# Kernel tuning notes

Hardware: AMD Instinct MI355X
Metric: run time of the kernel (lower is better)

Reference implementation:

```python
import jax, jax.numpy as jnp
import numpy as np

B, S, M, H = 4, 512, 128, 768
KEY_SIZE, VALUE_SIZE = 30000, 10000


def setup_inputs() -> dict:
    key = jax.random.key(0)
    k1, k2, k3, k4, k5, k6 = jax.random.split(key, 6)
    return {
        "word_seq": jax.random.randint(k1, (B, M), 0, KEY_SIZE),
        "hidden_state": jax.random.normal(k2, (B, S, H), dtype=jnp.float32),
        "label_value_matrix": jax.random.randint(k3, (B, S, M), 0, VALUE_SIZE),
        "word_mask_metrix": jax.random.uniform(k4, (B, S, M), dtype=jnp.float32),
        "key_table": jax.random.normal(k5, (KEY_SIZE, H), dtype=jnp.float32) * 0.02,
        "value_table": jax.random.normal(k6, (VALUE_SIZE, H), dtype=jnp.float32) * 0.02,
    }


def reference(word_seq, hidden_state, label_value_matrix, word_mask_metrix,
              key_table, value_table):
    temper = jnp.asarray(H, hidden_state.dtype) ** 0.5
    emb_a = key_table[word_seq]                      # [B, M, H]
    # u[b,s,m] = <hidden_state[b,s], emb_a[b,m]> / sqrt(H)
    u = jnp.einsum('bsh,bmh->bsm', hidden_state, emb_a) / temper
    mask = jnp.clip(word_mask_metrix, 0.0, 1.0)      # [B, S, M]
    delta_exp_u = jnp.exp(u) * mask                  # masked unnormalized attn
    p = delta_exp_u / (jnp.sum(delta_exp_u, axis=2, keepdims=True) + 1e-10)
    emb_c = value_table[label_value_matrix]          # [B, S, M, H]
    # o[b,s,h] = sum_m p[b,s,m] * emb_c[b,s,m,h]
    o = jnp.einsum('bsm,bsmh->bsh', p, emb_c)
    return o
```

## Files before the change

kernel.cpp:

```cpp
#include <hip/hip_runtime.h>
#include <hip/hip_bf16.h>


constexpr int B = 4, S = 512, M = 128, H = 768;
constexpr int C4 = H / 4;
constexpr int KEY_SIZE = 30000, VALUE_SIZE = 10000;

constexpr int VT_N = VALUE_SIZE * H;
constexpr int KA_N = B * M * H;
constexpr int HS_N = B * S * H;
constexpr int U_N  = B * S * M;

constexpr size_t VT_BYTES = (size_t)VT_N * 2;
constexpr size_t KA_BYTES = (size_t)KA_N * 2;
constexpr size_t HS_BYTES = (size_t)HS_N * 2;
constexpr size_t U_BYTES  = (size_t)U_N  * 4;
constexpr size_t WS_NEEDED = VT_BYTES + KA_BYTES + HS_BYTES + U_BYTES;

constexpr int VT_V4 = VT_N / 4, KA_V4 = KA_N / 4, HS_V4 = HS_N / 4;
constexpr int CONV_TOTAL = VT_V4 + KA_V4 + HS_V4;

typedef short  bf16x8  __attribute__((ext_vector_type(8)));
typedef float  floatx4 __attribute__((ext_vector_type(4)));

__device__ inline unsigned short f2bf(float f) {
    __hip_bfloat16 h = __float2bfloat16(f);
    return *reinterpret_cast<unsigned short*>(&h);
}
__device__ inline float bf2f(unsigned short u) {
    return __uint_as_float((unsigned)u << 16);
}
__device__ inline float4 bf4_to_f4(ushort4 u) {
    float4 f;
    f.x = bf2f(u.x); f.y = bf2f(u.y); f.z = bf2f(u.z); f.w = bf2f(u.w);
    return f;
}
__device__ inline ushort4 f4_to_bf4(float4 f) {
    ushort4 u; u.x = f2bf(f.x); u.y = f2bf(f.y); u.z = f2bf(f.z); u.w = f2bf(f.w);
    return u;
}

__global__ __launch_bounds__(256) void convert_kernel(
    const float* __restrict__ vt, const float* __restrict__ kt,
    const float* __restrict__ hs, const int* __restrict__ wseq,
    unsigned short* __restrict__ vt_bf, unsigned short* __restrict__ ka_bf,
    unsigned short* __restrict__ hs_bf)
{
    int i = blockIdx.x * 256 + threadIdx.x;
    if (i < VT_V4) {
        ((ushort4*)vt_bf)[i] = f4_to_bf4(((const float4*)vt)[i]);
    } else if (i < VT_V4 + KA_V4) {
        int j   = i - VT_V4;
        int c   = j % (H / 4);
        int row = j / (H / 4);
        int src = wseq[row];
        float4 f = ((const float4*)(kt + (size_t)src * H))[c];
        ((ushort4*)ka_bf)[j] = f4_to_bf4(f);
    } else if (i < CONV_TOTAL) {
        int j = i - VT_V4 - KA_V4;
        ((ushort4*)hs_bf)[j] = f4_to_bf4(((const float4*)hs)[j]);
    }
}

__global__ __launch_bounds__(256) void phaseA_kernel(
    const unsigned short* __restrict__ hs_bf,
    const unsigned short* __restrict__ ka_bf,
    float* __restrict__ u_ws)
{
    const int lane = threadIdx.x & 63;
    const int wave = threadIdx.x >> 6;
    const int tile = blockIdx.x * 4 + wave;
    const int b    = tile >> 8;
    const int r    = tile & 255;
    const int s0   = (r >> 3) << 4;
    const int m0   = (r & 7) << 4;
    const int l15  = lane & 15;
    const int quad = lane >> 4;

    const unsigned short* arow = hs_bf + (size_t)(b * S + s0 + l15) * H + quad * 8;
    const unsigned short* brow = ka_bf + (size_t)(b * M + m0 + l15) * H + quad * 8;

    floatx4 acc = {0.f, 0.f, 0.f, 0.f};
    #pragma unroll 4
    for (int k = 0; k < H; k += 32) {
        bf16x8 af = *(const bf16x8*)(arow + k);
        bf16x8 bf = *(const bf16x8*)(brow + k);
        acc = __builtin_amdgcn_mfma_f32_16x16x32_bf16(af, bf, acc, 0, 0, 0);
    }
    float* up = u_ws + (size_t)(b * S + s0 + quad * 4) * M + m0 + l15;
    up[0 * M] = acc[0];
    up[1 * M] = acc[1];
    up[2 * M] = acc[2];
    up[3 * M] = acc[3];
}

constexpr int GW = 6;
__global__ __launch_bounds__(384) void gather_kernel(
    const float* __restrict__ u_ws,
    const int*   __restrict__ lvm,
    const float* __restrict__ mask,
    const unsigned short* __restrict__ vt_bf,
    float*       __restrict__ out)
{
    const int bs   = blockIdx.x;
    const int t    = threadIdx.x;
    const int lane = t & 63;
    const int wave = t >> 6;

    __shared__ float  delta_s[M];
    __shared__ int    row_s[M];
    __shared__ float4 obuf[GW][C4];
    __shared__ float  dsum_s[GW];

    const float inv_temper = rsqrtf((float)H);
    if (t < M) {
        float u  = u_ws[(size_t)bs * M + t];
        float mk = mask[(size_t)bs * M + t];
        mk = fminf(fmaxf(mk, 0.f), 1.f);
        delta_s[t] = __expf(u * inv_temper) * mk;
        row_s[t]   = lvm[(size_t)bs * M + t];
    }
    __syncthreads();

    float4 a0 = {0.f,0.f,0.f,0.f}, a1 = {0.f,0.f,0.f,0.f}, a2 = {0.f,0.f,0.f,0.f};
    float dsum = 0.f;

    #pragma unroll 4
    for (int m = wave; m < M; m += GW) {
        const float pm = delta_s[m];
        const ushort4* vr = (const ushort4*)(vt_bf + (size_t)row_s[m] * H);
        const ushort4 vu0 = vr[lane];
        const ushort4 vu1 = vr[lane + 64];
        const ushort4 vu2 = vr[lane + 128];
        dsum += pm;
        const float4 v0 = bf4_to_f4(vu0);
        const float4 v1 = bf4_to_f4(vu1);
        const float4 v2 = bf4_to_f4(vu2);
        a0.x += pm*v0.x; a0.y += pm*v0.y; a0.z += pm*v0.z; a0.w += pm*v0.w;
        a1.x += pm*v1.x; a1.y += pm*v1.y; a1.z += pm*v1.z; a1.w += pm*v1.w;
        a2.x += pm*v2.x; a2.y += pm*v2.y; a2.z += pm*v2.z; a2.w += pm*v2.w;
    }

    obuf[wave][lane]       = a0;
    obuf[wave][lane + 64]  = a1;
    obuf[wave][lane + 128] = a2;
    if (lane == 0) dsum_s[wave] = dsum;
    __syncthreads();

    if (t < C4) {
        float d = 1e-10f;
        #pragma unroll
        for (int w = 0; w < GW; ++w) d += dsum_s[w];
        const float inv_d = 1.0f / d;
        float4 r = {0.f, 0.f, 0.f, 0.f};
        #pragma unroll
        for (int w = 0; w < GW; ++w) {
            const float4 o = obuf[w][t];
            r.x += o.x; r.y += o.y; r.z += o.z; r.w += o.w;
        }
        r.x *= inv_d; r.y *= inv_d; r.z *= inv_d; r.w *= inv_d;
        ((float4*)(out + (size_t)bs * H))[t] = r;
    }
}

__global__ __launch_bounds__(192) void kvmn_fp32_kernel(
    const int*   __restrict__ word_seq,
    const float* __restrict__ hidden_state,
    const int*   __restrict__ lvm,
    const float* __restrict__ mask,
    const float* __restrict__ key_table,
    const float* __restrict__ value_table,
    float*       __restrict__ out)
{
    const int bs   = blockIdx.x;
    const int b    = bs / S;
    const int t    = threadIdx.x;
    const int lane = t & 63;
    const int wave = t >> 6;

    __shared__ float4 hs4_s[C4];
    __shared__ int    wseq_s[M];
    __shared__ int    row_s[M];
    __shared__ float  mask_s[M];
    __shared__ float4 obuf[3][C4];
    __shared__ float  dsum_s[3];

    const float4* hs_g4 = (const float4*)(hidden_state + (size_t)bs * H);
    hs4_s[t] = hs_g4[t];
    if (t < M) {
        wseq_s[t] = word_seq[b * M + t];
        row_s[t]  = lvm[(size_t)bs * M + t];
        float mk  = mask[(size_t)bs * M + t];
        mask_s[t] = fminf(fmaxf(mk, 0.f), 1.f);
    }
    __syncthreads();

    const float4 h0 = hs4_s[lane];
    const float4 h1 = hs4_s[lane + 64];
    const float4 h2 = hs4_s[lane + 128];
    const float inv_temper = rsqrtf((float)H);
    const float4* kt4 = (const float4*)key_table;
    const float4* vt4 = (const float4*)value_table;

    float4 a0 = {0.f,0.f,0.f,0.f}, a1 = {0.f,0.f,0.f,0.f}, a2 = {0.f,0.f,0.f,0.f};
    float dsum = 0.f;

    #pragma unroll 2
    for (int m = wave; m < M; m += 3) {
        const float4* kr = kt4 + (size_t)wseq_s[m] * C4;
        const float4* vr = vt4 + (size_t)row_s[m]  * C4;
        const float4 k0 = kr[lane], k1 = kr[lane+64], k2 = kr[lane+128];
        const float4 v0 = vr[lane], v1 = vr[lane+64], v2 = vr[lane+128];
        float dot = h0.x*k0.x + h0.y*k0.y + h0.z*k0.z + h0.w*k0.w
                  + h1.x*k1.x + h1.y*k1.y + h1.z*k1.z + h1.w*k1.w
                  + h2.x*k2.x + h2.y*k2.y + h2.z*k2.z + h2.w*k2.w;
        #pragma unroll
        for (int off = 1; off < 64; off <<= 1) dot += __shfl_xor(dot, off);
        const float delta = __expf(dot * inv_temper) * mask_s[m];
        dsum += delta;
        a0.x += delta*v0.x; a0.y += delta*v0.y; a0.z += delta*v0.z; a0.w += delta*v0.w;
        a1.x += delta*v1.x; a1.y += delta*v1.y; a1.z += delta*v1.z; a1.w += delta*v1.w;
        a2.x += delta*v2.x; a2.y += delta*v2.y; a2.z += delta*v2.z; a2.w += delta*v2.w;
    }
    obuf[wave][lane] = a0; obuf[wave][lane+64] = a1; obuf[wave][lane+128] = a2;
    if (lane == 0) dsum_s[wave] = dsum;
    __syncthreads();
    const float inv_d = 1.0f / (dsum_s[0] + dsum_s[1] + dsum_s[2] + 1e-10f);
    const float4 r0 = obuf[0][t], r1 = obuf[1][t], r2 = obuf[2][t];
    float4 r;
    r.x = (r0.x+r1.x+r2.x)*inv_d; r.y = (r0.y+r1.y+r2.y)*inv_d;
    r.z = (r0.z+r1.z+r2.z)*inv_d; r.w = (r0.w+r1.w+r2.w)*inv_d;
    ((float4*)(out + (size_t)bs * H))[t] = r;
}

extern "C" void kernel_launch(void* const* d_in, const int* in_sizes, int n_in,
                              void* d_out, int out_size, void* d_ws, size_t ws_size,
                              hipStream_t stream) {
    const int*   word_seq    = (const int*)  d_in[0];
    const float* hidden      = (const float*)d_in[1];
    const int*   lvm         = (const int*)  d_in[2];
    const float* mask        = (const float*)d_in[3];
    const float* key_table   = (const float*)d_in[4];
    const float* value_table = (const float*)d_in[5];
    float* out = (float*)d_out;

    if (ws_size >= WS_NEEDED) {
        unsigned short* vt_bf = (unsigned short*)d_ws;
        unsigned short* ka_bf = (unsigned short*)((char*)d_ws + VT_BYTES);
        unsigned short* hs_bf = (unsigned short*)((char*)d_ws + VT_BYTES + KA_BYTES);
        float*          u_ws  = (float*)((char*)d_ws + VT_BYTES + KA_BYTES + HS_BYTES);

        convert_kernel<<<(CONV_TOTAL + 255) / 256, 256, 0, stream>>>(
            value_table, key_table, hidden, word_seq, vt_bf, ka_bf, hs_bf);
        phaseA_kernel<<<(B * S / 16) * (M / 16) / 4, 256, 0, stream>>>(
            hs_bf, ka_bf, u_ws);
        gather_kernel<<<B * S, 64 * GW, 0, stream>>>(
            u_ws, lvm, mask, vt_bf, out);
    } else {
        kvmn_fp32_kernel<<<B * S, 192, 0, stream>>>(
            word_seq, hidden, lvm, mask, key_table, value_table, out);
    }
}
```

Before: 206.3 us.

## Restructure gather kernel to 192 threads with 16-byte bf16 loads per lane

The value-gather kernel drops from six waves of 64 lanes to 192 threads, split into two halves of 96 lanes. Each lane loads 8 bf16 values (16 bytes) per row, and the halves alternate over the 128 rows. The denominator is now a separate wave shuffle reduction, and the two halves merge through a small shared buffer instead of a six-way reduction. The goal is wider loads and a cheaper reduction, at the cost of fewer waves per block to hide gather latency.

New measurement: 203.9 us. About the same (-1.2%).

```diff
diff --git a/kernel.cpp b/kernel.cpp
--- a/kernel.cpp
+++ b/kernel.cpp
@@ -20,8 +20,9 @@
 constexpr int VT_V4 = VT_N / 4, KA_V4 = KA_N / 4, HS_V4 = HS_N / 4;
 constexpr int CONV_TOTAL = VT_V4 + KA_V4 + HS_V4;
 
-typedef short  bf16x8  __attribute__((ext_vector_type(8)));
-typedef float  floatx4 __attribute__((ext_vector_type(4)));
+typedef short          bf16x8  __attribute__((ext_vector_type(8)));
+typedef float          floatx4 __attribute__((ext_vector_type(4)));
+typedef unsigned short ushort8v __attribute__((ext_vector_type(8)));
 
 __device__ inline unsigned short f2bf(float f) {
     __hip_bfloat16 h = __float2bfloat16(f);
@@ -29,11 +30,6 @@
 }
 __device__ inline float bf2f(unsigned short u) {
     return __uint_as_float((unsigned)u << 16);
-}
-__device__ inline float4 bf4_to_f4(ushort4 u) {
-    float4 f;
-    f.x = bf2f(u.x); f.y = bf2f(u.y); f.z = bf2f(u.z); f.w = bf2f(u.w);
-    return f;
 }
 __device__ inline ushort4 f4_to_bf4(float4 f) {
     ushort4 u; u.x = f2bf(f.x); u.y = f2bf(f.y); u.z = f2bf(f.z); u.w = f2bf(f.w);
@@ -94,23 +90,22 @@
     up[3 * M] = acc[3];
 }
 
-constexpr int GW = 6;
-__global__ __launch_bounds__(384) void gather_kernel(
+__global__ __launch_bounds__(192) void gather_kernel(
     const float* __restrict__ u_ws,
     const int*   __restrict__ lvm,
     const float* __restrict__ mask,
     const unsigned short* __restrict__ vt_bf,
     float*       __restrict__ out)
 {
-    const int bs   = blockIdx.x;
-    const int t    = threadIdx.x;
-    const int lane = t & 63;
-    const int wave = t >> 6;
-
-    __shared__ float  delta_s[M];
-    __shared__ int    row_s[M];
-    __shared__ float4 obuf[GW][C4];
-    __shared__ float  dsum_s[GW];
+    const int bs = blockIdx.x;
+    const int t  = threadIdx.x;
+    const int p  = t / 96;
+    const int c  = t - p * 96;
+
+    __shared__ float delta_s[M];
+    __shared__ int   row_s[M];
+    __shared__ float merge_s[8][100];
+    __shared__ float dsum_s;
 
     const float inv_temper = rsqrtf((float)H);
     if (t < M) {
@@ -122,44 +117,51 @@
     }
     __syncthreads();
 
-    float4 a0 = {0.f,0.f,0.f,0.f}, a1 = {0.f,0.f,0.f,0.f}, a2 = {0.f,0.f,0.f,0.f};
-    float dsum = 0.f;
-
-    #pragma unroll 4
-    for (int m = wave; m < M; m += GW) {
+    if (t < 64) {
+        float d = delta_s[t] + delta_s[t + 64];
+        #pragma unroll
+        for (int off = 1; off < 64; off <<= 1) d += __shfl_xor(d, off);
+        if (t == 0) dsum_s = d + 1e-10f;
+    }
+
+    float a0 = 0.f, a1 = 0.f, a2 = 0.f, a3 = 0.f;
+    float a4 = 0.f, a5 = 0.f, a6 = 0.f, a7 = 0.f;
+
+    const unsigned short* base = vt_bf + c * 8;
+    #pragma unroll 8
+    for (int m = p; m < M; m += 2) {
         const float pm = delta_s[m];
-        const ushort4* vr = (const ushort4*)(vt_bf + (size_t)row_s[m] * H);
-        const ushort4 vu0 = vr[lane];
-        const ushort4 vu1 = vr[lane + 64];
-        const ushort4 vu2 = vr[lane + 128];
-        dsum += pm;
-        const float4 v0 = bf4_to_f4(vu0);
-        const float4 v1 = bf4_to_f4(vu1);
-        const float4 v2 = bf4_to_f4(vu2);
-        a0.x += pm*v0.x; a0.y += pm*v0.y; a0.z += pm*v0.z; a0.w += pm*v0.w;
-        a1.x += pm*v1.x; a1.y += pm*v1.y; a1.z += pm*v1.z; a1.w += pm*v1.w;
-        a2.x += pm*v2.x; a2.y += pm*v2.y; a2.z += pm*v2.z; a2.w += pm*v2.w;
-    }
-
-    obuf[wave][lane]       = a0;
-    obuf[wave][lane + 64]  = a1;
-    obuf[wave][lane + 128] = a2;
-    if (lane == 0) dsum_s[wave] = dsum;
-    __syncthreads();
-
-    if (t < C4) {
-        float d = 1e-10f;
-        #pragma unroll
-        for (int w = 0; w < GW; ++w) d += dsum_s[w];
-        const float inv_d = 1.0f / d;
-        float4 r = {0.f, 0.f, 0.f, 0.f};
-        #pragma unroll
-        for (int w = 0; w < GW; ++w) {
-            const float4 o = obuf[w][t];
-            r.x += o.x; r.y += o.y; r.z += o.z; r.w += o.w;
-        }
-        r.x *= inv_d; r.y *= inv_d; r.z *= inv_d; r.w *= inv_d;
-        ((float4*)(out + (size_t)bs * H))[t] = r;
+        ushort8v v = *(const ushort8v*)(base + (size_t)row_s[m] * H);
+        a0 += pm * bf2f(v[0]);
+        a1 += pm * bf2f(v[1]);
+        a2 += pm * bf2f(v[2]);
+        a3 += pm * bf2f(v[3]);
+        a4 += pm * bf2f(v[4]);
+        a5 += pm * bf2f(v[5]);
+        a6 += pm * bf2f(v[6]);
+        a7 += pm * bf2f(v[7]);
+    }
+
+    if (p == 1) {
+        merge_s[0][c] = a0; merge_s[1][c] = a1; merge_s[2][c] = a2; merge_s[3][c] = a3;
+        merge_s[4][c] = a4; merge_s[5][c] = a5; merge_s[6][c] = a6; merge_s[7][c] = a7;
+    }
+    __syncthreads();
+
+    if (p == 0) {
+        const float inv_d = 1.0f / dsum_s;
+        float4 r0, r1;
+        r0.x = (a0 + merge_s[0][c]) * inv_d;
+        r0.y = (a1 + merge_s[1][c]) * inv_d;
+        r0.z = (a2 + merge_s[2][c]) * inv_d;
+        r0.w = (a3 + merge_s[3][c]) * inv_d;
+        r1.x = (a4 + merge_s[4][c]) * inv_d;
+        r1.y = (a5 + merge_s[5][c]) * inv_d;
+        r1.z = (a6 + merge_s[6][c]) * inv_d;
+        r1.w = (a7 + merge_s[7][c]) * inv_d;
+        float4* og = (float4*)(out + (size_t)bs * H + c * 8);
+        og[0] = r0;
+        og[1] = r1;
     }
 }
 
@@ -183,7 +185,7 @@
     __shared__ int    row_s[M];
     __shared__ float  mask_s[M];
     __shared__ float4 obuf[3][C4];
-    __shared__ float  dsum_s[3];
+    __shared__ float  dsum_s3[3];
 
     const float4* hs_g4 = (const float4*)(hidden_state + (size_t)bs * H);
     hs4_s[t] = hs_g4[t];
@@ -223,9 +225,9 @@
         a2.x += delta*v2.x; a2.y += delta*v2.y; a2.z += delta*v2.z; a2.w += delta*v2.w;
     }
     obuf[wave][lane] = a0; obuf[wave][lane+64] = a1; obuf[wave][lane+128] = a2;
-    if (lane == 0) dsum_s[wave] = dsum;
-    __syncthreads();
-    const float inv_d = 1.0f / (dsum_s[0] + dsum_s[1] + dsum_s[2] + 1e-10f);
+    if (lane == 0) dsum_s3[wave] = dsum;
+    __syncthreads();
+    const float inv_d = 1.0f / (dsum_s3[0] + dsum_s3[1] + dsum_s3[2] + 1e-10f);
     const float4 r0 = obuf[0][t], r1 = obuf[1][t], r2 = obuf[2][t];
     float4 r;
     r.x = (r0.x+r1.x+r2.x)*inv_d; r.y = (r0.y+r1.y+r2.y)*inv_d;
@@ -254,7 +256,7 @@
             value_table, key_table, hidden, word_seq, vt_bf, ka_bf, hs_bf);
         phaseA_kernel<<<(B * S / 16) * (M / 16) / 4, 256, 0, stream>>>(
             hs_bf, ka_bf, u_ws);
-        gather_kernel<<<B * S, 64 * GW, 0, stream>>>(
+        gather_kernel<<<B * S, 192, 0, stream>>>(
             u_ws, lvm, mask, vt_bf, out);
     } else {
         kvmn_fp32_kernel<<<B * S, 192, 0, stream>>>(
```
